# Kernel optimization log

Hardware: AMD Instinct MI355X
Metric: run time of the kernel (lower is better)

## Reference

```python
import jax, jax.numpy as jnp
import numpy as np

B, T, D_IN, E, H = 2, 2048, 1024, 64, 16  # batch, num_tokens, input dim, emb_size(per-head), num_heads


def setup_inputs() -> dict:
    key = jax.random.key(0)
    ks = jax.random.split(key, 6)
    s = 0.02
    inp = jax.random.normal(ks[0], (B, T, D_IN), dtype=jnp.float32)
    # causal mask: 1.0 where attention is disallowed (j > i), matching `scaled_compat -= mask * 1e9`
    mask = jnp.triu(jnp.ones((T, T), dtype=jnp.float32), k=1)
    Wq = jax.random.normal(ks[1], (D_IN, E * H), dtype=jnp.float32) * s
    Wk = jax.random.normal(ks[2], (D_IN, E * H), dtype=jnp.float32) * s
    Wv = jax.random.normal(ks[3], (D_IN, E * H), dtype=jnp.float32) * s
    Wu = jax.random.normal(ks[4], (E * H, E), dtype=jnp.float32) * s
    bu = jnp.zeros((E,), dtype=jnp.float32)
    return {"inp": inp, "mask": mask, "Wq": Wq, "Wk": Wk, "Wv": Wv, "Wu": Wu, "bu": bu}


def reference(inp, mask, Wq, Wk, Wv, Wu, bu):
    b = inp.shape[0]
    q = inp @ Wq  # [B,T,E*H]
    k = inp @ Wk
    v = inp @ Wv
    # NOTE: original reshapes last dim as (E, H) -> heads on fastest axis (interleaved layout)
    q = q.reshape(b, T, E, H)
    k = k.reshape(b, T, E, H)
    v = v.reshape(b, T, E, H)
    scores = jnp.einsum("bteh,bseh->bhts", q, k) / jnp.sqrt(jnp.float32(E))  # [B,H,T,T]
    if mask is not None:
        scores = scores - mask * 1e9
    attn = jax.nn.softmax(scores, axis=-1)
    wv = jnp.einsum("bhts,bseh->bhte", attn, v)  # [B,H,T,E]
    # transpose [0,2,3,1] -> [B,T,E,H], then flatten to [B,T,E*H] (H fastest, matching original)
    wv = jnp.transpose(wv, (0, 2, 3, 1)).reshape(b, T, E * H)
    return wv @ Wu + bu  # unify Dense(emb_size), with bias
```

## Files before the change

### kernel.cpp

```cpp
#include <hip/hip_runtime.h>


typedef __bf16 bf16x8 __attribute__((ext_vector_type(8)));
typedef float f32x4 __attribute__((ext_vector_type(4)));
typedef unsigned short u16;
typedef unsigned int u32;

#define AS1 __attribute__((address_space(1)))
#define AS3 __attribute__((address_space(3)))

__device__ __forceinline__ void gll16(const void* g, void* l) {
    __builtin_amdgcn_global_load_lds((const AS1 u32*)g, (AS3 u32*)l, 16, 0, 0);
}

__device__ __forceinline__ u16 f2bf(float f) {
    union { float f; u32 u; } v; v.f = f;
    u32 r = (v.u + 0x7FFFu + ((v.u >> 16) & 1u)) >> 16;
    return (u16)r;
}

#define MM 4096
#define SCALE_LOG2E 0.18033688011112042f

__global__ void cast_x(const float* __restrict__ in, u16* __restrict__ out, int n4) {
    int i = blockIdx.x * blockDim.x + threadIdx.x;
    if (i < n4) {
        float4 f = ((const float4*)in)[i];
        ushort4 o;
        o.x = f2bf(f.x); o.y = f2bf(f.y); o.z = f2bf(f.z); o.w = f2bf(f.w);
        ((ushort4*)out)[i] = o;
    }
}

__global__ void transpose_w(const float* __restrict__ Wq, const float* __restrict__ Wk,
                            const float* __restrict__ Wv, const float* __restrict__ Wu,
                            u16* __restrict__ wqt, u16* __restrict__ wkt,
                            u16* __restrict__ wvt, u16* __restrict__ wut) {
    int z = blockIdx.z;
    const float* src; u16* dst; int N;
    if (z == 0)      { src = Wq; dst = wqt; N = 1024; }
    else if (z == 1) { src = Wk; dst = wkt; N = 1024; }
    else if (z == 2) { src = Wv; dst = wvt; N = 1024; }
    else             { src = Wu; dst = wut; N = 64; if (blockIdx.y >= 2) return; }
    __shared__ float lds[32][33];
    int k0 = blockIdx.x * 32, n0 = blockIdx.y * 32;
    int tid = threadIdx.x;
    int c = tid & 31, r0 = tid >> 5;
#pragma unroll
    for (int p = 0; p < 4; ++p) {
        int r = r0 + p * 8;
        lds[r][c] = src[(k0 + r) * N + n0 + c];
    }
    __syncthreads();
#pragma unroll
    for (int p = 0; p < 4; ++p) {
        int n = n0 + r0 + p * 8;
        if (z < 3) {
            int rnew = ((n & 15) << 6) | (n >> 4);
            dst[rnew * 1024 + k0 + c] = f2bf(lds[c][n - n0]);
        } else {
            int k = k0 + c;
            int kp = ((k & 15) << 6) | (k >> 4);
            dst[n * 1024 + kp] = f2bf(lds[c][n - n0]);
        }
    }
}

__global__ __launch_bounds__(256) void gemm_qkv(const u16* __restrict__ xb,
                                                const u16* __restrict__ wqt,
                                                const u16* __restrict__ wkt,
                                                const u16* __restrict__ wvt,
                                                u16* __restrict__ qh, u16* __restrict__ kh,
                                                u16* __restrict__ vh) {
    int z = blockIdx.z;
    const u16* wt = (z == 0) ? wqt : (z == 1) ? wkt : wvt;
    u16* dst      = (z == 0) ? qh  : (z == 1) ? kh  : vh;
    __shared__ u16 lA[2][128 * 32];
    __shared__ u16 lB[2][128 * 32];
    int tid = threadIdx.x;
    int m0 = blockIdx.x * 128, n0 = blockIdx.y * 128;
    int lane = tid & 63, w = tid >> 6;
    int wr = w >> 1, wc = w & 1;
    int l15 = lane & 15, quad = lane >> 4;
    f32x4 acc[4][4] = {};
    int srow = tid >> 2, scol = (tid & 3) * 8;
    const u16* ga = xb + (m0 + srow) * 1024 + scol;
    const u16* gb = wt + (n0 + srow) * 1024 + scol;
#pragma unroll
    for (int pp = 0; pp < 2; ++pp) {
        gll16(ga + pp * 65536, lA[0] + (pp * 256 + tid) * 8);
        gll16(gb + pp * 65536, lB[0] + (pp * 256 + tid) * 8);
    }
#pragma unroll 1
    for (int kk = 0; kk < 32; ++kk) {
        int cur = kk & 1;
        asm volatile("s_waitcnt vmcnt(0)" ::: "memory");
        __builtin_amdgcn_s_barrier();
        if (kk + 1 < 32) {
            int kb = (kk + 1) * 32;
#pragma unroll
            for (int pp = 0; pp < 2; ++pp) {
                gll16(ga + pp * 65536 + kb, lA[cur ^ 1] + (pp * 256 + tid) * 8);
                gll16(gb + pp * 65536 + kb, lB[cur ^ 1] + (pp * 256 + tid) * 8);
            }
        }
        bf16x8 af[4], bfr[4];
#pragma unroll
        for (int i = 0; i < 4; ++i)
            af[i] = *(const bf16x8*)(lA[cur] + (wr * 64 + i * 16 + l15) * 32 + quad * 8);
#pragma unroll
        for (int j = 0; j < 4; ++j)
            bfr[j] = *(const bf16x8*)(lB[cur] + (wc * 64 + j * 16 + l15) * 32 + quad * 8);
#pragma unroll
        for (int i = 0; i < 4; ++i)
#pragma unroll
            for (int j = 0; j < 4; ++j)
                acc[i][j] = __builtin_amdgcn_mfma_f32_16x16x32_bf16(af[i], bfr[j], acc[i][j], 0, 0, 0);
    }
    int bb = m0 >> 11;
    int hb = (n0 >> 6) + wc;
    if (z < 2) {
        float scale = (z == 0) ? SCALE_LOG2E : 1.f;
#pragma unroll
        for (int i = 0; i < 4; ++i)
#pragma unroll
            for (int j = 0; j < 4; ++j)
#pragma unroll
                for (int r = 0; r < 4; ++r) {
                    int m = m0 + wr * 64 + i * 16 + quad * 4 + r;
                    dst[m * 1024 + hb * 64 + j * 16 + l15] = f2bf(acc[i][j][r] * scale);
                }
    } else {
#pragma unroll
        for (int i = 0; i < 4; ++i)
#pragma unroll
            for (int j = 0; j < 4; ++j) {
                int t4 = (m0 & 2047) + wr * 64 + i * 16 + quad * 4;
                ushort4 o;
                o.x = f2bf(acc[i][j][0]); o.y = f2bf(acc[i][j][1]);
                o.z = f2bf(acc[i][j][2]); o.w = f2bf(acc[i][j][3]);
                *(ushort4*)(dst + (((bb * 16 + hb) * 64) + j * 16 + l15) * 2048 + t4) = o;
            }
    }
}

__global__ __launch_bounds__(256, 8) void attn(const u16* __restrict__ qh, const u16* __restrict__ kh,
                                               const u16* __restrict__ vh, u16* __restrict__ ot,
                                               float* __restrict__ part, float* __restrict__ lp) {
    __shared__ u16 smem[12800];
    u16* sQ = smem;
    u16* sK = smem + 4608;
    u16* sV = smem + 8704;
    const int tid = threadIdx.x;
    const int lane = tid & 63, w = tid >> 6;
    const int quad = lane >> 4, l15 = lane & 15;
    const int s = blockIdx.x, by = blockIdx.y;
    int qt, j0, j1, half;
    if (s < 16)      { qt = 15 - s;  j0 = 0;             j1 = qt + 1;        half = -1; }
    else if (s < 32) { qt = s;       j0 = 0;             j1 = (qt + 1) >> 1; half = 0;  }
    else             { qt = s - 16;  j0 = (qt + 1) >> 1; j1 = qt + 1;        half = 1;  }
    const int b = by >> 4, h = by & 15;
    const u16* qbase = qh + (b * 2048) * 1024 + h * 64;
    const u16* kbase = kh + (b * 2048) * 1024 + h * 64;
    const u16* vbase = vh + (by * 64) * 2048;
    const int c0 = tid, c1 = 256 + tid;
    const int r0c = c0 >> 3, o0c = (c0 & 7) * 8;
    const int r1c = c1 >> 3, o1c = (c1 & 7) * 8;
    const int sw0 = ((r0c >> 1) & 3) << 3;
    const int sw1 = ((r1c >> 1) & 3) << 3;
    u16* sKd0 = sK + (o0c >> 5) * 2048 + r0c * 32 + ((o0c & 31) ^ sw0);
    u16* sKd1 = sK + (o1c >> 5) * 2048 + r1c * 32 + ((o1c & 31) ^ sw1);
    u16* sVd0 = sV + (o0c >> 5) * 2048 + r0c * 32 + ((o0c & 31) ^ sw0);
    u16* sVd1 = sV + (o1c >> 5) * 2048 + r1c * 32 + ((o1c & 31) ^ sw1);
    const u16* kg0 = kbase + r0c * 1024 + o0c;
    const u16* kg1 = kbase + r1c * 1024 + o1c;
    const u16* vg0 = vbase + r0c * 2048 + o0c;
    const u16* vg1 = vbase + r1c * 2048 + o1c;
    const int qsw = (quad ^ ((l15 >> 1) & 3)) * 8;

    gll16(qbase + (qt * 64 + r0c) * 1024 + o0c, sQ + c0 * 8);
    gll16(qbase + (qt * 64 + r1c) * 1024 + o1c, sQ + c1 * 8);
    __syncthreads();
    bf16x8 aq[2];
    aq[0] = *(const bf16x8*)(sQ + (w * 16 + l15) * 64 + quad * 8);
    aq[1] = *(const bf16x8*)(sQ + (w * 16 + l15) * 64 + 32 + quad * 8);
    float lpart[4] = {0.f, 0.f, 0.f, 0.f};
    f32x4 oacc[4] = {};
    uint4 kr0 = *(const uint4*)(kg0 + j0 * 65536);
    uint4 kr1 = *(const uint4*)(kg1 + j0 * 65536);
    uint4 vr0 = *(const uint4*)(vg0 + j0 * 64);
    uint4 vr1 = *(const uint4*)(vg1 + j0 * 64);
    for (int jt = j0; jt < j1; ++jt) {
        __syncthreads();
        *(uint4*)sKd0 = kr0; *(uint4*)sKd1 = kr1;
        *(uint4*)sVd0 = vr0; *(uint4*)sVd1 = vr1;
        __syncthreads();
        if (jt + 1 < j1) {
            kr0 = *(const uint4*)(kg0 + (jt + 1) * 65536);
            kr1 = *(const uint4*)(kg1 + (jt + 1) * 65536);
            vr0 = *(const uint4*)(vg0 + (jt + 1) * 64);
            vr1 = *(const uint4*)(vg1 + (jt + 1) * 64);
        }
        f32x4 sacc[4] = {};
#pragma unroll
        for (int j4 = 0; j4 < 4; ++j4)
#pragma unroll
            for (int k2 = 0; k2 < 2; ++k2) {
                bf16x8 bk = *(const bf16x8*)(sK + k2 * 2048 + (j4 * 16 + l15) * 32 + qsw);
                sacc[j4] = __builtin_amdgcn_mfma_f32_16x16x32_bf16(aq[k2], bk, sacc[j4], 0, 0, 0);
            }
        if (jt == qt) {
#pragma unroll
            for (int j4 = 0; j4 < 4; ++j4)
#pragma unroll
                for (int r = 0; r < 4; ++r) {
                    int sg = j4 * 16 + l15;
                    int tg = w * 16 + quad * 4 + r;
                    if (sg > tg) sacc[j4][r] = -1e30f;
                }
        }
#pragma unroll
        for (int j4 = 0; j4 < 4; ++j4)
#pragma unroll
            for (int r = 0; r < 4; ++r) {
                float pe = __builtin_amdgcn_exp2f(sacc[j4][r]);
                sacc[j4][r] = pe;
                lpart[r] += pe;
            }
        u16* sP = sQ;
#pragma unroll
        for (int j4 = 0; j4 < 4; ++j4)
#pragma unroll
            for (int r = 0; r < 4; ++r)
                sP[(w * 16 + quad * 4 + r) * 72 + j4 * 16 + l15] = f2bf(sacc[j4][r]);
        bf16x8 ap[2];
        ap[0] = *(const bf16x8*)(sP + (w * 16 + l15) * 72 + quad * 8);
        ap[1] = *(const bf16x8*)(sP + (w * 16 + l15) * 72 + 32 + quad * 8);
#pragma unroll
        for (int e4 = 0; e4 < 4; ++e4)
#pragma unroll
            for (int k2 = 0; k2 < 2; ++k2) {
                bf16x8 bv = *(const bf16x8*)(sV + k2 * 2048 + (e4 * 16 + l15) * 32 + qsw);
                oacc[e4] = __builtin_amdgcn_mfma_f32_16x16x32_bf16(ap[k2], bv, oacc[e4], 0, 0, 0);
            }
    }
    if (half < 0) {
#pragma unroll
        for (int r = 0; r < 4; ++r) {
            float rs = lpart[r];
#pragma unroll
            for (int off = 1; off < 16; off <<= 1) rs += __shfl_xor(rs, off, 16);
            float inv = 1.f / rs;
            int t = qt * 64 + w * 16 + quad * 4 + r;
            int base = (b * 2048 + t) * 1024 + h * 64;
#pragma unroll
            for (int e4 = 0; e4 < 4; ++e4)
                ot[base + e4 * 16 + l15] = f2bf(oacc[e4][r] * inv);
        }
    } else {
        int pb = by * 16 + (qt - 16);
        float* pg = part + (pb * 2 + half) * 4096;
        float* lg = lp + pb * 128 + half * 64;
#pragma unroll
        for (int r = 0; r < 4; ++r) {
            float rs = lpart[r];
#pragma unroll
            for (int off = 1; off < 16; off <<= 1) rs += __shfl_xor(rs, off, 16);
            int row = w * 16 + quad * 4 + r;
            if (l15 == 0) lg[row] = rs;
#pragma unroll
            for (int e4 = 0; e4 < 4; ++e4)
                pg[row * 64 + e4 * 16 + l15] = oacc[e4][r];
        }
    }
}

__global__ __launch_bounds__(256) void combine_o(const float* __restrict__ part,
                                                 const float* __restrict__ lp,
                                                 u16* __restrict__ ot) {
    int pb = blockIdx.x, tid = threadIdx.x;
    int by = pb >> 4, qt = 16 + (pb & 15);
    int b = by >> 4, h = by & 15;
    const float* pA = part + pb * 8192;
    const float* pB = pA + 4096;
    const float* lA = lp + pb * 128;
    const float* lB = lA + 64;
#pragma unroll
    for (int p = 0; p < 4; ++p) {
        int e = p * 1024 + tid * 4;
        int row = e >> 6, col = e & 63;
        float4 a = *(const float4*)(pA + e);
        float4 c = *(const float4*)(pB + e);
        float inv = 1.f / (lA[row] + lB[row]);
        int t = qt * 64 + row;
        ushort4 o;
        o.x = f2bf((a.x + c.x) * inv); o.y = f2bf((a.y + c.y) * inv);
        o.z = f2bf((a.z + c.z) * inv); o.w = f2bf((a.w + c.w) * inv);
        *(ushort4*)(ot + (b * 2048 + t) * 1024 + h * 64 + col) = o;
    }
}

__global__ __launch_bounds__(256) void gemm_out(const u16* __restrict__ ot, const u16* __restrict__ wut,
                                                const float* __restrict__ bu, float* __restrict__ out) {
    __shared__ float red[4][1088];
    int tid = threadIdx.x, lane = tid & 63, w = tid >> 6;
    int quad = lane >> 4, l15 = lane & 15;
    int m0 = blockIdx.x * 16;
    f32x4 acc[4] = {};
    const u16* aptr = ot + (m0 + l15) * 1024 + w * 256 + quad * 8;
    const u16* bptr = wut + l15 * 1024 + w * 256 + quad * 8;
#pragma unroll
    for (int kk = 0; kk < 8; ++kk) {
        bf16x8 af = *(const bf16x8*)(aptr + kk * 32);
#pragma unroll
        for (int j = 0; j < 4; ++j) {
            bf16x8 bfr = *(const bf16x8*)(bptr + j * 16 * 1024 + kk * 32);
            acc[j] = __builtin_amdgcn_mfma_f32_16x16x32_bf16(af, bfr, acc[j], 0, 0, 0);
        }
    }
#pragma unroll
    for (int j = 0; j < 4; ++j)
#pragma unroll
        for (int r = 0; r < 4; ++r)
            red[w][(j * 16 + l15) * 17 + quad * 4 + r] = acc[j][r];
    __syncthreads();
    int n = tid & 63, mq = tid >> 6;
    float bias = bu[n];
#pragma unroll
    for (int i = 0; i < 4; ++i) {
        int m = mq * 4 + i;
        float s = red[0][n * 17 + m] + red[1][n * 17 + m] + red[2][n * 17 + m] + red[3][n * 17 + m];
        out[(m0 + m) * 64 + n] = s + bias;
    }
}

#define OFF_XB   0u
#define OFF_WQT  8388608u
#define OFF_WKT  10485760u
#define OFF_WVT  12582912u
#define OFF_WUT  14680064u
#define OFF_QH   14811136u
#define OFF_KH   23199744u
#define OFF_VH   31588352u
#define OFF_OT   OFF_XB
#define OFF_PART 39976960u
#define OFF_LP   56754176u

extern "C" void kernel_launch(void* const* d_in, const int* in_sizes, int n_in,
                              void* d_out, int out_size, void* d_ws, size_t ws_size,
                              hipStream_t stream) {
    (void)in_sizes; (void)n_in; (void)out_size; (void)ws_size;
    const float* inp = (const float*)d_in[0];
    const float* Wq = (const float*)d_in[2];
    const float* Wk = (const float*)d_in[3];
    const float* Wv = (const float*)d_in[4];
    const float* Wu = (const float*)d_in[5];
    const float* bu = (const float*)d_in[6];
    float* out = (float*)d_out;
    char* ws = (char*)d_ws;
    u16* xb  = (u16*)(ws + OFF_XB);
    u16* wqt = (u16*)(ws + OFF_WQT);
    u16* wkt = (u16*)(ws + OFF_WKT);
    u16* wvt = (u16*)(ws + OFF_WVT);
    u16* wut = (u16*)(ws + OFF_WUT);
    u16* qh  = (u16*)(ws + OFF_QH);
    u16* kh  = (u16*)(ws + OFF_KH);
    u16* vh  = (u16*)(ws + OFF_VH);
    u16* ot  = (u16*)(ws + OFF_OT);
    float* part = (float*)(ws + OFF_PART);
    float* lpw  = (float*)(ws + OFF_LP);

    cast_x<<<4096, 256, 0, stream>>>(inp, xb, (MM * 1024) / 4);
    transpose_w<<<dim3(32, 32, 4), 256, 0, stream>>>(Wq, Wk, Wv, Wu, wqt, wkt, wvt, wut);
    gemm_qkv<<<dim3(32, 8, 3), 256, 0, stream>>>(xb, wqt, wkt, wvt, qh, kh, vh);
    attn<<<dim3(48, 32), 256, 0, stream>>>(qh, kh, vh, ot, part, lpw);
    combine_o<<<512, 256, 0, stream>>>(part, lpw, ot);
    gemm_out<<<256, 256, 0, stream>>>(ot, wut, bu, out);
}
```

Measured before the change: 193.8 us.

## Double attention query tile to 128 rows and permute V layout for vectorized P stores

The attention kernel now gives each block 128 query rows, two 16-row groups per wave, instead of 64. Each K/V tile loaded into shared memory therefore feeds twice as many MFMAs. The causal split scheme, partial buffers and combine kernel are resized to match. The V output of the QKV GEMM is written with a permuted token order, so each lane can store P as one ushort4 and the V operand stays consistent with that order. In exchange the grid halves, the occupancy hint is dropped, and each block uses more registers and LDS, which may lower parallelism.

```diff
diff --git a/kernel.cpp b/kernel.cpp
--- a/kernel.cpp
+++ b/kernel.cpp
@@ -132,35 +132,34 @@
                 }
     } else {
 #pragma unroll
-        for (int i = 0; i < 4; ++i)
-#pragma unroll
-            for (int j = 0; j < 4; ++j) {
-                int t4 = (m0 & 2047) + wr * 64 + i * 16 + quad * 4;
+        for (int j = 0; j < 4; ++j)
+#pragma unroll
+            for (int r = 0; r < 4; ++r) {
                 ushort4 o;
-                o.x = f2bf(acc[i][j][0]); o.y = f2bf(acc[i][j][1]);
-                o.z = f2bf(acc[i][j][2]); o.w = f2bf(acc[i][j][3]);
-                *(ushort4*)(dst + (((bb * 16 + hb) * 64) + j * 16 + l15) * 2048 + t4) = o;
-            }
-    }
-}
-
-__global__ __launch_bounds__(256, 8) void attn(const u16* __restrict__ qh, const u16* __restrict__ kh,
-                                               const u16* __restrict__ vh, u16* __restrict__ ot,
-                                               float* __restrict__ part, float* __restrict__ lp) {
-    __shared__ u16 smem[12800];
-    u16* sQ = smem;
-    u16* sK = smem + 4608;
-    u16* sV = smem + 8704;
+                o.x = f2bf(acc[0][j][r]); o.y = f2bf(acc[1][j][r]);
+                o.z = f2bf(acc[2][j][r]); o.w = f2bf(acc[3][j][r]);
+                *(ushort4*)(dst + (((bb * 16 + hb) * 64) + j * 16 + l15) * 2048 +
+                            (m0 & 2047) + wr * 64 + (quad * 4 + r) * 4) = o;
+            }
+    }
+}
+
+__global__ __launch_bounds__(256) void attn(const u16* __restrict__ qh, const u16* __restrict__ kh,
+                                            const u16* __restrict__ vh, u16* __restrict__ ot,
+                                            float* __restrict__ part, float* __restrict__ lp) {
+    __shared__ u16 smem[17408];
+    u16* sPQ = smem;
+    u16* sK = smem + 9216;
+    u16* sV = smem + 13312;
     const int tid = threadIdx.x;
     const int lane = tid & 63, w = tid >> 6;
     const int quad = lane >> 4, l15 = lane & 15;
     const int s = blockIdx.x, by = blockIdx.y;
     int qt, j0, j1, half;
-    if (s < 16)      { qt = 15 - s;  j0 = 0;             j1 = qt + 1;        half = -1; }
-    else if (s < 32) { qt = s;       j0 = 0;             j1 = (qt + 1) >> 1; half = 0;  }
-    else             { qt = s - 16;  j0 = (qt + 1) >> 1; j1 = qt + 1;        half = 1;  }
+    if (s < 8)       { qt = 7 - s;  j0 = 0;      j1 = 2 * qt + 2; half = -1; }
+    else if (s < 16) { qt = s;      j0 = 0;      j1 = qt + 1;     half = 0;  }
+    else             { qt = s - 8;  j0 = qt + 1; j1 = 2 * qt + 2; half = 1;  }
     const int b = by >> 4, h = by & 15;
-    const u16* qbase = qh + (b * 2048) * 1024 + h * 64;
     const u16* kbase = kh + (b * 2048) * 1024 + h * 64;
     const u16* vbase = vh + (by * 64) * 2048;
     const int c0 = tid, c1 = 256 + tid;
@@ -178,18 +177,27 @@
     const u16* vg1 = vbase + r1c * 2048 + o1c;
     const int qsw = (quad ^ ((l15 >> 1) & 3)) * 8;
 
-    gll16(qbase + (qt * 64 + r0c) * 1024 + o0c, sQ + c0 * 8);
-    gll16(qbase + (qt * 64 + r1c) * 1024 + o1c, sQ + c1 * 8);
+    const u16* qg = qh + (b * 2048 + qt * 128) * 1024 + h * 64;
+#pragma unroll
+    for (int p = 0; p < 4; ++p) {
+        int c = p * 256 + tid;
+        gll16(qg + (c >> 3) * 1024 + (c & 7) * 8, sPQ + c * 8);
+    }
     __syncthreads();
-    bf16x8 aq[2];
-    aq[0] = *(const bf16x8*)(sQ + (w * 16 + l15) * 64 + quad * 8);
-    aq[1] = *(const bf16x8*)(sQ + (w * 16 + l15) * 64 + 32 + quad * 8);
-    float lpart[4] = {0.f, 0.f, 0.f, 0.f};
-    f32x4 oacc[4] = {};
+    bf16x8 aq[2][2];
+#pragma unroll
+    for (int rg = 0; rg < 2; ++rg)
+#pragma unroll
+        for (int k2 = 0; k2 < 2; ++k2)
+            aq[rg][k2] = *(const bf16x8*)(sPQ + (w * 32 + rg * 16 + l15) * 64 + k2 * 32 + quad * 8);
+
+    float lpart[2][4] = {};
+    f32x4 oacc[2][4] = {};
     uint4 kr0 = *(const uint4*)(kg0 + j0 * 65536);
     uint4 kr1 = *(const uint4*)(kg1 + j0 * 65536);
     uint4 vr0 = *(const uint4*)(vg0 + j0 * 64);
     uint4 vr1 = *(const uint4*)(vg1 + j0 * 64);
+    u16* sPw = sPQ + w * 2304;
     for (int jt = j0; jt < j1; ++jt) {
         __syncthreads();
         *(uint4*)sKd0 = kr0; *(uint4*)sKd1 = kr1;
@@ -201,77 +209,94 @@
             vr0 = *(const uint4*)(vg0 + (jt + 1) * 64);
             vr1 = *(const uint4*)(vg1 + (jt + 1) * 64);
         }
-        f32x4 sacc[4] = {};
+        f32x4 sacc[2][4] = {};
 #pragma unroll
         for (int j4 = 0; j4 < 4; ++j4)
 #pragma unroll
             for (int k2 = 0; k2 < 2; ++k2) {
                 bf16x8 bk = *(const bf16x8*)(sK + k2 * 2048 + (j4 * 16 + l15) * 32 + qsw);
-                sacc[j4] = __builtin_amdgcn_mfma_f32_16x16x32_bf16(aq[k2], bk, sacc[j4], 0, 0, 0);
-            }
-        if (jt == qt) {
+                sacc[0][j4] = __builtin_amdgcn_mfma_f32_16x16x32_bf16(aq[0][k2], bk, sacc[0][j4], 0, 0, 0);
+                sacc[1][j4] = __builtin_amdgcn_mfma_f32_16x16x32_bf16(aq[1][k2], bk, sacc[1][j4], 0, 0, 0);
+            }
+        if (jt >= 2 * qt) {
+            int soff = (jt - 2 * qt) * 64;
+#pragma unroll
+            for (int rg = 0; rg < 2; ++rg)
+#pragma unroll
+                for (int j4 = 0; j4 < 4; ++j4)
+#pragma unroll
+                    for (int r = 0; r < 4; ++r) {
+                        int sg = soff + j4 * 16 + l15;
+                        int tg = w * 32 + rg * 16 + quad * 4 + r;
+                        if (sg > tg) sacc[rg][j4][r] = -1e30f;
+                    }
+        }
+#pragma unroll
+        for (int rg = 0; rg < 2; ++rg)
 #pragma unroll
             for (int j4 = 0; j4 < 4; ++j4)
 #pragma unroll
                 for (int r = 0; r < 4; ++r) {
-                    int sg = j4 * 16 + l15;
-                    int tg = w * 16 + quad * 4 + r;
-                    if (sg > tg) sacc[j4][r] = -1e30f;
+                    float pe = __builtin_amdgcn_exp2f(sacc[rg][j4][r]);
+                    sacc[rg][j4][r] = pe;
+                    lpart[rg][r] += pe;
                 }
-        }
-#pragma unroll
-        for (int j4 = 0; j4 < 4; ++j4)
+#pragma unroll
+        for (int rg = 0; rg < 2; ++rg)
 #pragma unroll
             for (int r = 0; r < 4; ++r) {
-                float pe = __builtin_amdgcn_exp2f(sacc[j4][r]);
-                sacc[j4][r] = pe;
-                lpart[r] += pe;
-            }
-        u16* sP = sQ;
-#pragma unroll
-        for (int j4 = 0; j4 < 4; ++j4)
-#pragma unroll
-            for (int r = 0; r < 4; ++r)
-                sP[(w * 16 + quad * 4 + r) * 72 + j4 * 16 + l15] = f2bf(sacc[j4][r]);
-        bf16x8 ap[2];
-        ap[0] = *(const bf16x8*)(sP + (w * 16 + l15) * 72 + quad * 8);
-        ap[1] = *(const bf16x8*)(sP + (w * 16 + l15) * 72 + 32 + quad * 8);
+                ushort4 o;
+                o.x = f2bf(sacc[rg][0][r]); o.y = f2bf(sacc[rg][1][r]);
+                o.z = f2bf(sacc[rg][2][r]); o.w = f2bf(sacc[rg][3][r]);
+                *(ushort4*)(sPw + (rg * 16 + quad * 4 + r) * 72 + l15 * 4) = o;
+            }
+        bf16x8 ap[2][2];
+#pragma unroll
+        for (int rg = 0; rg < 2; ++rg)
+#pragma unroll
+            for (int k2 = 0; k2 < 2; ++k2)
+                ap[rg][k2] = *(const bf16x8*)(sPw + (rg * 16 + l15) * 72 + k2 * 32 + quad * 8);
 #pragma unroll
         for (int e4 = 0; e4 < 4; ++e4)
 #pragma unroll
             for (int k2 = 0; k2 < 2; ++k2) {
                 bf16x8 bv = *(const bf16x8*)(sV + k2 * 2048 + (e4 * 16 + l15) * 32 + qsw);
-                oacc[e4] = __builtin_amdgcn_mfma_f32_16x16x32_bf16(ap[k2], bv, oacc[e4], 0, 0, 0);
+                oacc[0][e4] = __builtin_amdgcn_mfma_f32_16x16x32_bf16(ap[0][k2], bv, oacc[0][e4], 0, 0, 0);
+                oacc[1][e4] = __builtin_amdgcn_mfma_f32_16x16x32_bf16(ap[1][k2], bv, oacc[1][e4], 0, 0, 0);
             }
     }
     if (half < 0) {
 #pragma unroll
-        for (int r = 0; r < 4; ++r) {
-            float rs = lpart[r];
-#pragma unroll
-            for (int off = 1; off < 16; off <<= 1) rs += __shfl_xor(rs, off, 16);
-            float inv = 1.f / rs;
-            int t = qt * 64 + w * 16 + quad * 4 + r;
-            int base = (b * 2048 + t) * 1024 + h * 64;
-#pragma unroll
-            for (int e4 = 0; e4 < 4; ++e4)
-                ot[base + e4 * 16 + l15] = f2bf(oacc[e4][r] * inv);
-        }
+        for (int rg = 0; rg < 2; ++rg)
+#pragma unroll
+            for (int r = 0; r < 4; ++r) {
+                float rs = lpart[rg][r];
+#pragma unroll
+                for (int off = 1; off < 16; off <<= 1) rs += __shfl_xor(rs, off, 16);
+                float inv = 1.f / rs;
+                int t = qt * 128 + w * 32 + rg * 16 + quad * 4 + r;
+                int base = (b * 2048 + t) * 1024 + h * 64;
+#pragma unroll
+                for (int e4 = 0; e4 < 4; ++e4)
+                    ot[base + e4 * 16 + l15] = f2bf(oacc[rg][e4][r] * inv);
+            }
     } else {
-        int pb = by * 16 + (qt - 16);
-        float* pg = part + (pb * 2 + half) * 4096;
-        float* lg = lp + pb * 128 + half * 64;
-#pragma unroll
-        for (int r = 0; r < 4; ++r) {
-            float rs = lpart[r];
-#pragma unroll
-            for (int off = 1; off < 16; off <<= 1) rs += __shfl_xor(rs, off, 16);
-            int row = w * 16 + quad * 4 + r;
-            if (l15 == 0) lg[row] = rs;
-#pragma unroll
-            for (int e4 = 0; e4 < 4; ++e4)
-                pg[row * 64 + e4 * 16 + l15] = oacc[e4][r];
-        }
+        int pb = by * 8 + (qt - 8);
+        float* pg = part + (pb * 2 + half) * 8192;
+        float* lg = lp + pb * 256 + half * 128;
+#pragma unroll
+        for (int rg = 0; rg < 2; ++rg)
+#pragma unroll
+            for (int r = 0; r < 4; ++r) {
+                float rs = lpart[rg][r];
+#pragma unroll
+                for (int off = 1; off < 16; off <<= 1) rs += __shfl_xor(rs, off, 16);
+                int row = w * 32 + rg * 16 + quad * 4 + r;
+                if (l15 == 0) lg[row] = rs;
+#pragma unroll
+                for (int e4 = 0; e4 < 4; ++e4)
+                    pg[row * 64 + e4 * 16 + l15] = oacc[rg][e4][r];
+            }
     }
 }
 
@@ -279,20 +304,20 @@
                                                  const float* __restrict__ lp,
                                                  u16* __restrict__ ot) {
     int pb = blockIdx.x, tid = threadIdx.x;
-    int by = pb >> 4, qt = 16 + (pb & 15);
+    int by = pb >> 3, qt = 8 + (pb & 7);
     int b = by >> 4, h = by & 15;
-    const float* pA = part + pb * 8192;
-    const float* pB = pA + 4096;
-    const float* lA = lp + pb * 128;
-    const float* lB = lA + 64;
-#pragma unroll
-    for (int p = 0; p < 4; ++p) {
+    const float* pA = part + pb * 16384;
+    const float* pB = pA + 8192;
+    const float* lA = lp + pb * 256;
+    const float* lB = lA + 128;
+#pragma unroll
+    for (int p = 0; p < 8; ++p) {
         int e = p * 1024 + tid * 4;
         int row = e >> 6, col = e & 63;
         float4 a = *(const float4*)(pA + e);
         float4 c = *(const float4*)(pB + e);
         float inv = 1.f / (lA[row] + lB[row]);
-        int t = qt * 64 + row;
+        int t = qt * 128 + row;
         ushort4 o;
         o.x = f2bf((a.x + c.x) * inv); o.y = f2bf((a.y + c.y) * inv);
         o.z = f2bf((a.z + c.z) * inv); o.w = f2bf((a.w + c.w) * inv);
@@ -373,7 +398,7 @@
     cast_x<<<4096, 256, 0, stream>>>(inp, xb, (MM * 1024) / 4);
     transpose_w<<<dim3(32, 32, 4), 256, 0, stream>>>(Wq, Wk, Wv, Wu, wqt, wkt, wvt, wut);
     gemm_qkv<<<dim3(32, 8, 3), 256, 0, stream>>>(xb, wqt, wkt, wvt, qh, kh, vh);
-    attn<<<dim3(48, 32), 256, 0, stream>>>(qh, kh, vh, ot, part, lpw);
-    combine_o<<<512, 256, 0, stream>>>(part, lpw, ot);
+    attn<<<dim3(24, 32), 256, 0, stream>>>(qh, kh, vh, ot, part, lpw);
+    combine_o<<<256, 256, 0, stream>>>(part, lpw, ot);
     gemm_out<<<256, 256, 0, stream>>>(ot, wut, bu, out);
 }
```

Result: no change. 195.4 us (+0.8%).
